# Optimization experiments

Hardware: AMD Instinct MI355X
Metric: run time of the kernel (lower is better)

The kernel has to match this reference:

```python
import jax, jax.numpy as jnp
import numpy as np

D_MODEL = 1024
N_HEADS = 16
N_KV = 4
GROUPS = N_HEADS // N_KV  # 4
D_K = D_MODEL // N_HEADS  # 64
ROPE_BASE = 10000.0
SCALE = float(np.sqrt(D_K))


def rope_cos_sin(T):
    # standard RoPE tables: [T, D_K]
    inv_freq = 1.0 / (ROPE_BASE ** (jnp.arange(0, D_K, 2, dtype=jnp.float32) / D_K))
    t = jnp.arange(T, dtype=jnp.float32)
    freqs = jnp.outer(t, inv_freq)                      # [T, D_K/2]
    emb = jnp.concatenate([freqs, freqs], axis=-1)      # [T, D_K]
    return jnp.cos(emb), jnp.sin(emb)


def apply_rope(x, cos, sin):
    # x: [B, H, T, D_K]; cos/sin: [T, D_K]
    x1, x2 = jnp.split(x, 2, axis=-1)
    rot = jnp.concatenate([-x2, x1], axis=-1)
    return x * cos[None, None] + rot * sin[None, None]


def setup_inputs() -> dict:
    key = jax.random.key(0)
    ks = jax.random.split(key, 7)
    B, T = 2, 2048
    w = lambda k, shape: jax.random.normal(k, shape, jnp.float32) * 0.02
    return {
        "q": jax.random.normal(ks[0], (B, T, D_MODEL), jnp.float32),
        "k": jax.random.normal(ks[1], (B, T, D_MODEL), jnp.float32),
        "v": jax.random.normal(ks[2], (B, T, D_MODEL), jnp.float32),
        "W_q": w(ks[3], (D_MODEL, N_HEADS * D_K)),
        "W_k": w(ks[4], (D_MODEL, N_KV * D_K)),
        "W_v": w(ks[5], (D_MODEL, N_KV * D_K)),
        "W_o": w(ks[6], (D_MODEL, D_MODEL)),
    }


def reference(q, k, v, W_q, W_k, W_v, W_o):
    B, T_q, _ = q.shape
    T_k = k.shape[1]
    # projections -> [B, H, T, D_K] (repeat_interleave == reshape heads as (kv, group))
    Q = (q @ W_q).reshape(B, T_q, N_HEADS, D_K).transpose(0, 2, 1, 3)
    K = (k @ W_k).reshape(B, T_k, N_KV, D_K).transpose(0, 2, 1, 3)
    V = (v @ W_v).reshape(B, T_k, N_KV, D_K).transpose(0, 2, 1, 3)
    cos_q, sin_q = rope_cos_sin(T_q)
    cos_k, sin_k = rope_cos_sin(T_k)
    Q = apply_rope(Q, cos_q, sin_q)
    K = apply_rope(K, cos_k, sin_k)
    # group query heads per kv head: [B, N_KV, GROUPS, T_q, D_K] (no K/V duplication)
    Qg = Q.reshape(B, N_KV, GROUPS, T_q, D_K)
    scores = jnp.einsum('bkgqd,bkld->bkgql', Qg, K) / SCALE  # [B,N_KV,G,T_q,T_k]
    attn = jax.nn.softmax(scores, axis=-1)
    out = jnp.einsum('bkgql,bkld->bkgqd', attn, V)           # [B,N_KV,G,T_q,D_K]
    out = out.reshape(B, N_HEADS, T_q, D_K).transpose(0, 2, 1, 3).reshape(B, T_q, N_HEADS * D_K)
    return out @ W_o
```

## Files before the change

kernel.cpp:

```cpp
#include <hip/hip_runtime.h>
#include <hip/hip_bf16.h>
#include <math.h>

#define B_ 2
#define T_ 2048
#define DM_ 1024
#define NH_ 16
#define NKV_ 4
#define G_ 4
#define DK_ 64
#define SCL 0.1803368784f

#define BAR_LG()                                              \
  do {                                                        \
    asm volatile("s_waitcnt lgkmcnt(0)" ::: "memory");        \
    __builtin_amdgcn_s_barrier();                             \
  } while (0)

typedef __attribute__((ext_vector_type(8))) short bf16x8;
typedef __attribute__((ext_vector_type(4))) float f32x4;
typedef __attribute__((ext_vector_type(16))) float f32x16;
typedef __attribute__((ext_vector_type(8))) unsigned short u16x8;
typedef __attribute__((ext_vector_type(4))) unsigned short u16x4;

static __device__ __forceinline__ ushort f2bf(float x) {
  __hip_bfloat16 h = __float2bfloat16(x);
  return *reinterpret_cast<ushort*>(&h);
}

__global__ __launch_bounds__(256) void prep_kernel(const float* __restrict__ Wq,
                                                   const float* __restrict__ Wk,
                                                   const float* __restrict__ Wv,
                                                   const float* __restrict__ Wo,
                                                   ushort* __restrict__ WtAll,
                                                   ushort* __restrict__ Wot,
                                                   float* __restrict__ cos_t,
                                                   float* __restrict__ sin_t) {
  const int tid = threadIdx.x;
  int bid = blockIdx.x;
  if (bid < 256) {
    int idx = bid * 256 + tid;
    int t = idx >> 5, i = idx & 31;
    float invf = 1.0f / powf(10000.0f, (float)i / 32.0f);
    float ang = (float)t * invf;
    cos_t[idx] = cosf(ang);
    sin_t[idx] = sinf(ang);
    return;
  }
  bid -= 256;
  const float* W; ushort* Wt; int N, bx, by;
  if (bid < 256)      { W = Wq; Wt = WtAll;                       N = 1024; bx = bid & 15;        by = bid >> 4; }
  else if (bid < 320) { W = Wk; Wt = WtAll + (size_t)1024 * 1024; N = 256;  bx = (bid - 256) & 3; by = (bid - 256) >> 2; }
  else if (bid < 384) { W = Wv; Wt = WtAll + (size_t)1280 * 1024; N = 256;  bx = (bid - 320) & 3; by = (bid - 320) >> 2; }
  else                { W = Wo; Wt = Wot;                         N = 1024; bx = (bid - 384) & 15; by = (bid - 384) >> 4; }
  const int n0 = bx * 64, k0 = by * 64;
  __shared__ float tile[64 * 65];
#pragma unroll
  for (int it = 0; it < 4; ++it) {
    int lin = tid + it * 256;
    int r = lin >> 4, c4 = lin & 15;
    float4 v = *(const float4*)(W + (size_t)(k0 + r) * N + n0 + c4 * 4);
    tile[r * 65 + c4 * 4 + 0] = v.x;
    tile[r * 65 + c4 * 4 + 1] = v.y;
    tile[r * 65 + c4 * 4 + 2] = v.z;
    tile[r * 65 + c4 * 4 + 3] = v.w;
  }
  __syncthreads();
#pragma unroll
  for (int it = 0; it < 4; ++it) {
    int lin = tid + it * 256;
    int n = lin >> 4, c4 = lin & 15;
    u16x4 o;
#pragma unroll
    for (int j = 0; j < 4; ++j) o[j] = f2bf(tile[(c4 * 4 + j) * 65 + n]);
    *(u16x4*)(Wt + (size_t)(n0 + n) * 1024 + k0 + c4 * 4) = o;
  }
}

__global__ __launch_bounds__(256, 2) void bgemm_kernel(const float* __restrict__ Aq,
                                                       const float* __restrict__ Ak,
                                                       const float* __restrict__ Av,
                                                       const ushort* __restrict__ Abf,
                                                       const ushort* __restrict__ Bt,
                                                       ushort* __restrict__ Qb,
                                                       ushort* __restrict__ Kb,
                                                       ushort* __restrict__ Vt,
                                                       float* __restrict__ Of, int mode,
                                                       const float* __restrict__ cos_t,
                                                       const float* __restrict__ sin_t) {
  const int tid = threadIdx.x;
  const int w = tid >> 6, lane = tid & 63;
  const int lr = lane & 15, lg = lane >> 4;
  const int wm = w >> 1, wn = w & 1;
  const int n0 = blockIdx.x * 128;
  const int m0 = blockIdx.y * 64;
  const bool f32A = (mode != 3);
  const float* Af = (n0 < 1024) ? Aq : (n0 < 1280 ? Ak : Av);

  __shared__ __align__(16) ushort As[64 * 64];
  __shared__ __align__(16) ushort Bs[128 * 64];

  f32x4 acc[2][4];
#pragma unroll
  for (int mt = 0; mt < 2; ++mt)
#pragma unroll
    for (int nt = 0; nt < 4; ++nt) acc[mt][nt] = (f32x4){0.f, 0.f, 0.f, 0.f};

  const int sr = tid >> 3, sch = tid & 7;

  float4 apf[2][2];
  u16x8 apb[2];
  u16x8 bpf[4];
  if (f32A) {
#pragma unroll
    for (int it = 0; it < 2; ++it) {
      int r = sr + it * 32;
      apf[it][0] = *(const float4*)(Af + (size_t)(m0 + r) * 1024 + sch * 8);
      apf[it][1] = *(const float4*)(Af + (size_t)(m0 + r) * 1024 + sch * 8 + 4);
    }
  } else {
#pragma unroll
    for (int it = 0; it < 2; ++it) {
      int r = sr + it * 32;
      apb[it] = *(const u16x8*)(Abf + (size_t)(m0 + r) * 1024 + sch * 8);
    }
  }
#pragma unroll
  for (int it = 0; it < 4; ++it) {
    int r = sr + it * 32;
    bpf[it] = *(const u16x8*)(Bt + (size_t)(n0 + r) * 1024 + sch * 8);
  }

  for (int kt = 0; kt < 16; ++kt) {
    BAR_LG();
#pragma unroll
    for (int it = 0; it < 2; ++it) {
      int r = sr + it * 32;
      int byte = (r * 128 + sch * 16) ^ ((r & 7) << 4);
      u16x8 aw;
      if (f32A) {
        aw[0] = f2bf(apf[it][0].x); aw[1] = f2bf(apf[it][0].y);
        aw[2] = f2bf(apf[it][0].z); aw[3] = f2bf(apf[it][0].w);
        aw[4] = f2bf(apf[it][1].x); aw[5] = f2bf(apf[it][1].y);
        aw[6] = f2bf(apf[it][1].z); aw[7] = f2bf(apf[it][1].w);
      } else {
        aw = apb[it];
      }
      *(u16x8*)((char*)As + byte) = aw;
    }
#pragma unroll
    for (int it = 0; it < 4; ++it) {
      int r = sr + it * 32;
      int byte = (r * 128 + sch * 16) ^ ((r & 7) << 4);
      *(u16x8*)((char*)Bs + byte) = bpf[it];
    }
    BAR_LG();

    if (kt + 1 < 16) {
      if (f32A) {
#pragma unroll
        for (int it = 0; it < 2; ++it) {
          int r = sr + it * 32;
          apf[it][0] = *(const float4*)(Af + (size_t)(m0 + r) * 1024 + (kt + 1) * 64 + sch * 8);
          apf[it][1] = *(const float4*)(Af + (size_t)(m0 + r) * 1024 + (kt + 1) * 64 + sch * 8 + 4);
        }
      } else {
#pragma unroll
        for (int it = 0; it < 2; ++it) {
          int r = sr + it * 32;
          apb[it] = *(const u16x8*)(Abf + (size_t)(m0 + r) * 1024 + (kt + 1) * 64 + sch * 8);
        }
      }
#pragma unroll
      for (int it = 0; it < 4; ++it) {
        int r = sr + it * 32;
        bpf[it] = *(const u16x8*)(Bt + (size_t)(n0 + r) * 1024 + (kt + 1) * 64 + sch * 8);
      }
    }

    __builtin_amdgcn_s_setprio(1);
#pragma unroll
    for (int kc = 0; kc < 2; ++kc) {
      bf16x8 af[2], bfr[4];
#pragma unroll
      for (int mt = 0; mt < 2; ++mt) {
        int row = wm * 32 + mt * 16 + lr;
        int byte = (row * 128 + kc * 64 + lg * 16) ^ ((row & 7) << 4);
        af[mt] = *(bf16x8*)((char*)As + byte);
      }
#pragma unroll
      for (int nt = 0; nt < 4; ++nt) {
        int row = wn * 64 + nt * 16 + lr;
        int byte = (row * 128 + kc * 64 + lg * 16) ^ ((row & 7) << 4);
        bfr[nt] = *(bf16x8*)((char*)Bs + byte);
      }
#pragma unroll
      for (int mt = 0; mt < 2; ++mt)
#pragma unroll
        for (int nt = 0; nt < 4; ++nt)
          acc[mt][nt] = __builtin_amdgcn_mfma_f32_16x16x32_bf16(af[mt], bfr[nt], acc[mt][nt], 0, 0, 0);
    }
    __builtin_amdgcn_s_setprio(0);
  }

  const int colbase = n0 + wn * 64;
  if (mode == 3) {
#pragma unroll
    for (int mt = 0; mt < 2; ++mt) {
      int rbase = m0 + wm * 32 + mt * 16 + lg * 4;
#pragma unroll
      for (int r = 0; r < 4; ++r)
#pragma unroll
        for (int nt = 0; nt < 4; ++nt)
          Of[(size_t)(rbase + r) * DM_ + colbase + nt * 16 + lr] = acc[mt][nt][r];
    }
  } else if (colbase >= 1280) {
    int cb = colbase - 1280;
    int kvh = cb >> 6;
#pragma unroll
    for (int mt = 0; mt < 2; ++mt) {
      int row0 = m0 + wm * 32 + mt * 16 + lg * 4;
      int b = row0 >> 11, t0r = row0 & (T_ - 1);
#pragma unroll
      for (int nt = 0; nt < 4; ++nt) {
        int d = nt * 16 + lr;
        u16x4 o;
#pragma unroll
        for (int r = 0; r < 4; ++r) o[r] = f2bf(acc[mt][nt][r]);
        *(u16x4*)(Vt + ((size_t)(b * NKV_ + kvh) * DK_ + d) * T_ + t0r) = o;
      }
    }
  } else {
    const bool isQ = (colbase < 1024);
    const int cb = isQ ? colbase : (colbase - 1024);
    const int heads = isQ ? NH_ : NKV_;
    const float scl = isQ ? SCL : 1.0f;
    const int h = cb >> 6;
    ushort* O = isQ ? Qb : Kb;
#pragma unroll
    for (int mt = 0; mt < 2; ++mt) {
      int rbase = m0 + wm * 32 + mt * 16 + lg * 4;
#pragma unroll
      for (int r = 0; r < 4; ++r) {
        int row = rbase + r;
        int b = row >> 11, t = row & (T_ - 1);
#pragma unroll
        for (int nt = 0; nt < 2; ++nt) {
          int d = nt * 16 + lr;
          float c = cos_t[t * 32 + d], s = sin_t[t * 32 + d];
          float x1 = acc[mt][nt][r], x2 = acc[mt][nt + 2][r];
          size_t base = (((size_t)(b * heads + h)) * T_ + t) * DK_ + d;
          O[base] = f2bf((x1 * c - x2 * s) * scl);
          O[base + 32] = f2bf((x2 * c + x1 * s) * scl);
        }
      }
    }
  }
}

__global__ __launch_bounds__(128, 2) void attn_mfma_kernel(const ushort* __restrict__ Qb,
                                                           const ushort* __restrict__ Kb,
                                                           const ushort* __restrict__ Vt,
                                                           ushort* __restrict__ attn_out) {
  const int bid = blockIdx.x;
  const int gw = (bid & 7) * 128 + (bid >> 3);
  const int hb = gw >> 5;
  const int qt = gw & 31;
  const int b = hb >> 4;
  const int kv = (hb >> 2) & 3;
  const int g = hb & 3;
  const int h = kv * G_ + g;
  const int q0 = qt * 64;

  const int tid = threadIdx.x;
  const int w = tid >> 6;
  const int lane = tid & 63;
  const int l31 = lane & 31;
  const int hh = lane >> 5;

  __shared__ __align__(16) ushort Ks[2][64 * 64];
  __shared__ __align__(16) ushort Vs[2][64 * 64];

  const ushort* Qg = Qb + ((size_t)(b * NH_ + h) * T_ + q0 + w * 32) * DK_;
  const ushort* Kg = Kb + (size_t)(b * NKV_ + kv) * T_ * DK_;
  const ushort* Vg = Vt + (size_t)(b * NKV_ + kv) * DK_ * T_;

  bf16x8 aq[4];
#pragma unroll
  for (int ks = 0; ks < 4; ++ks)
    aq[ks] = *(const bf16x8*)(Qg + (size_t)l31 * DK_ + ks * 16 + hh * 8);

  f32x16 oacc0{}, oacc1{};
  float l_run = 0.f;

  const int sr = tid >> 3, sch = tid & 7;
  const int vcol0b = 8 * (sch & 1) + 32 * (sch >> 1);
  u16x8 kreg[4], vreg[4];

#define LOADT(t)                                                                    \
  {                                                                                 \
    _Pragma("unroll") for (int it = 0; it < 4; ++it) {                              \
      int r = sr + it * 16;                                                         \
      kreg[it] = *(const u16x8*)(Kg + (size_t)((t) * 64 + r) * DK_ + sch * 8);      \
      vreg[it] = *(const u16x8*)(Vg + (size_t)r * T_ + (t) * 64 + sch * 8);         \
    }                                                                               \
  }
#define STAGEW(bufi)                                                                \
  {                                                                                 \
    _Pragma("unroll") for (int it = 0; it < 4; ++it) {                              \
      int r = sr + it * 16;                                                         \
      int swz = (r & 7) << 4;                                                       \
      *(u16x8*)((char*)Ks[bufi] + ((r * 128 + sch * 16) ^ swz)) = kreg[it];         \
      int vx = (r * 128 + vcol0b) ^ swz;                                            \
      u16x4 lo, hi;                                                                 \
      _Pragma("unroll") for (int j = 0; j < 4; ++j) { lo[j] = vreg[it][j]; hi[j] = vreg[it][4 + j]; } \
      *(u16x4*)((char*)Vs[bufi] + vx) = lo;                                         \
      *(u16x4*)((char*)Vs[bufi] + (vx ^ 16)) = hi;                                  \
    }                                                                               \
  }

  LOADT(0);
  STAGEW(0);
  LOADT(1);
  __syncthreads();

  const int swf = (l31 & 7) << 4;

  for (int kt = 0; kt < T_ / 64; ++kt) {
    const int cur = kt & 1;
    if (kt + 1 < T_ / 64) STAGEW(cur ^ 1);
    if (kt + 2 < T_ / 64) LOADT(kt + 2);

    f32x16 st0{}, st1{};
    __builtin_amdgcn_s_setprio(1);
#pragma unroll
    for (int ks = 0; ks < 4; ++ks) {
      bf16x8 ak0 = *(bf16x8*)((char*)Ks[cur] + ((l31 * 128 + ks * 32 + hh * 16) ^ swf));
      bf16x8 ak1 = *(bf16x8*)((char*)Ks[cur] + (((32 + l31) * 128 + ks * 32 + hh * 16) ^ swf));
      st0 = __builtin_amdgcn_mfma_f32_32x32x16_bf16(ak0, aq[ks], st0, 0, 0, 0);
      st1 = __builtin_amdgcn_mfma_f32_32x32x16_bf16(ak1, aq[ks], st1, 0, 0, 0);
    }
    __builtin_amdgcn_s_setprio(0);

    float ps = 0.f;
#pragma unroll
    for (int r = 0; r < 16; ++r) {
      st0[r] = __builtin_amdgcn_exp2f(st0[r]);
      st1[r] = __builtin_amdgcn_exp2f(st1[r]);
      ps += st0[r] + st1[r];
    }
    l_run += ps;

    __builtin_amdgcn_s_setprio(1);
#pragma unroll
    for (int s = 0; s < 4; ++s) {
      const int base = (s & 1) * 8;
      u16x8 pw;
#pragma unroll
      for (int j = 0; j < 8; ++j)
        pw[j] = f2bf((s < 2) ? st0[base + j] : st1[base + j]);
      bf16x8 pa = *(bf16x8*)&pw;
      bf16x8 bv0 = *(bf16x8*)((char*)Vs[cur] + ((l31 * 128 + s * 32 + hh * 16) ^ swf));
      bf16x8 bv1 = *(bf16x8*)((char*)Vs[cur] + (((32 + l31) * 128 + s * 32 + hh * 16) ^ swf));
      oacc0 = __builtin_amdgcn_mfma_f32_32x32x16_bf16(pa, bv0, oacc0, 0, 0, 0);
      oacc1 = __builtin_amdgcn_mfma_f32_32x32x16_bf16(pa, bv1, oacc1, 0, 0, 0);
    }
    __builtin_amdgcn_s_setprio(0);

    __syncthreads();
  }

  float l_tot = l_run + __shfl_xor(l_run, 32, 64);
  float inv = 1.0f / l_tot;
#pragma unroll
  for (int r = 0; r < 16; ++r) {
    int qr = (r & 3) + 8 * (r >> 2) + 4 * hh;
    float ir = __shfl(inv, qr, 64);
    int t = q0 + w * 32 + qr;
    size_t base = ((size_t)b * T_ + t) * DM_ + h * DK_;
    attn_out[base + l31] = f2bf(oacc0[r] * ir);
    attn_out[base + 32 + l31] = f2bf(oacc1[r] * ir);
  }
#undef LOADT
#undef STAGEW
}

extern "C" void kernel_launch(void* const* d_in, const int* in_sizes, int n_in,
                              void* d_out, int out_size, void* d_ws, size_t ws_size,
                              hipStream_t stream) {
  const float* q  = (const float*)d_in[0];
  const float* k  = (const float*)d_in[1];
  const float* v  = (const float*)d_in[2];
  const float* Wq = (const float*)d_in[3];
  const float* Wk = (const float*)d_in[4];
  const float* Wv = (const float*)d_in[5];
  const float* Wo = (const float*)d_in[6];
  float* out = (float*)d_out;

  char* ws = (char*)d_ws;
  size_t off = 0;
  float* cos_t  = (float*)(ws + off);  off += (size_t)T_ * 32 * 4;
  float* sin_t  = (float*)(ws + off);  off += (size_t)T_ * 32 * 4;
  ushort* Ab    = (ushort*)(ws + off); off += (size_t)4096 * 1024 * 2;
  ushort* WtAll = (ushort*)(ws + off); off += (size_t)1536 * 1024 * 2;
  ushort* Wot   = (ushort*)(ws + off); off += (size_t)1024 * 1024 * 2;
  ushort* Qb    = (ushort*)(ws + off); off += (size_t)B_ * NH_ * T_ * DK_ * 2;
  ushort* Kb    = (ushort*)(ws + off); off += (size_t)B_ * NKV_ * T_ * DK_ * 2;
  ushort* Vt    = (ushort*)(ws + off); off += (size_t)B_ * NKV_ * T_ * DK_ * 2;

  prep_kernel<<<dim3(896), dim3(256), 0, stream>>>(Wq, Wk, Wv, Wo, WtAll, Wot, cos_t, sin_t);

  bgemm_kernel<<<dim3(12, 64), dim3(256), 0, stream>>>(q, k, v, nullptr, WtAll,
                                                       Qb, Kb, Vt, nullptr, 5, cos_t, sin_t);

  attn_mfma_kernel<<<dim3(1024), dim3(128), 0, stream>>>(Qb, Kb, Vt, Ab);

  bgemm_kernel<<<dim3(8, 64), dim3(256), 0, stream>>>(nullptr, nullptr, nullptr, Ab, Wot,
                                                      nullptr, nullptr, nullptr, out, 3, cos_t, sin_t);
}
```

Baseline: 112.8 us.

## Stream GEMM B tiles and attention K/V tiles directly into LDS via global_load_lds

Replaces the register-staged global→LDS copies with asynchronous global_load_lds (direct-to-LDS) loads. This applies to the weight tile in the projection GEMM, now double-buffered, and to the K/V tiles in the attention kernel. The XOR swizzle on those LDS buffers is dropped, since direct loads write contiguous rows. The V-transpose store permutes its lane groups so the memory layout matches the un-swizzled read pattern. The aim is to cut VGPR pressure and VALU/ds_write work for staging. The cost is possible LDS bank conflicts on reads and a shallower prefetch depth in attention (one tile instead of two).

```diff
diff --git a/kernel.cpp b/kernel.cpp
--- a/kernel.cpp
+++ b/kernel.cpp
@@ -16,6 +16,11 @@
     asm volatile("s_waitcnt lgkmcnt(0)" ::: "memory");        \
     __builtin_amdgcn_s_barrier();                             \
   } while (0)
+
+#define GLOAD16(gp, lp)                                                      \
+  __builtin_amdgcn_global_load_lds(                                          \
+      (const __attribute__((address_space(1))) unsigned int*)(gp),           \
+      (__attribute__((address_space(3))) unsigned int*)(lp), 16, 0, 0)
 
 typedef __attribute__((ext_vector_type(8))) short bf16x8;
 typedef __attribute__((ext_vector_type(4))) float f32x4;
@@ -96,9 +101,10 @@
   const int m0 = blockIdx.y * 64;
   const bool f32A = (mode != 3);
   const float* Af = (n0 < 1024) ? Aq : (n0 < 1280 ? Ak : Av);
+  const int krow8 = lane >> 3, kch = lane & 7;
 
   __shared__ __align__(16) ushort As[64 * 64];
-  __shared__ __align__(16) ushort Bs[128 * 64];
+  __shared__ __align__(16) ushort Bs[2][128 * 64];
 
   f32x4 acc[2][4];
 #pragma unroll
@@ -107,10 +113,16 @@
     for (int nt = 0; nt < 4; ++nt) acc[mt][nt] = (f32x4){0.f, 0.f, 0.f, 0.f};
 
   const int sr = tid >> 3, sch = tid & 7;
+
+#define ISSUE_B(bufi, t)                                                          \
+  {                                                                               \
+    _Pragma("unroll") for (int i = 0; i < 4; ++i)                                 \
+      GLOAD16(Bt + (size_t)(n0 + w * 32 + i * 8 + krow8) * 1024 + (t) * 64 + kch * 8, \
+              (char*)Bs[bufi] + (w * 32 + i * 8) * 128);                          \
+  }
 
   float4 apf[2][2];
   u16x8 apb[2];
-  u16x8 bpf[4];
   if (f32A) {
 #pragma unroll
     for (int it = 0; it < 2; ++it) {
@@ -125,14 +137,12 @@
       apb[it] = *(const u16x8*)(Abf + (size_t)(m0 + r) * 1024 + sch * 8);
     }
   }
-#pragma unroll
-  for (int it = 0; it < 4; ++it) {
-    int r = sr + it * 32;
-    bpf[it] = *(const u16x8*)(Bt + (size_t)(n0 + r) * 1024 + sch * 8);
-  }
+  ISSUE_B(0, 0);
 
   for (int kt = 0; kt < 16; ++kt) {
-    BAR_LG();
+    const int cur = kt & 1;
+    __syncthreads();
+    if (kt + 1 < 16) ISSUE_B(cur ^ 1, kt + 1);
 #pragma unroll
     for (int it = 0; it < 2; ++it) {
       int r = sr + it * 32;
@@ -148,12 +158,6 @@
       }
       *(u16x8*)((char*)As + byte) = aw;
     }
-#pragma unroll
-    for (int it = 0; it < 4; ++it) {
-      int r = sr + it * 32;
-      int byte = (r * 128 + sch * 16) ^ ((r & 7) << 4);
-      *(u16x8*)((char*)Bs + byte) = bpf[it];
-    }
     BAR_LG();
 
     if (kt + 1 < 16) {
@@ -171,11 +175,6 @@
           apb[it] = *(const u16x8*)(Abf + (size_t)(m0 + r) * 1024 + (kt + 1) * 64 + sch * 8);
         }
       }
-#pragma unroll
-      for (int it = 0; it < 4; ++it) {
-        int r = sr + it * 32;
-        bpf[it] = *(const u16x8*)(Bt + (size_t)(n0 + r) * 1024 + (kt + 1) * 64 + sch * 8);
-      }
     }
 
     __builtin_amdgcn_s_setprio(1);
@@ -191,8 +190,7 @@
 #pragma unroll
       for (int nt = 0; nt < 4; ++nt) {
         int row = wn * 64 + nt * 16 + lr;
-        int byte = (row * 128 + kc * 64 + lg * 16) ^ ((row & 7) << 4);
-        bfr[nt] = *(bf16x8*)((char*)Bs + byte);
+        bfr[nt] = *(bf16x8*)((char*)Bs[cur] + row * 128 + kc * 64 + lg * 16);
       }
 #pragma unroll
       for (int mt = 0; mt < 2; ++mt)
@@ -202,6 +200,7 @@
     }
     __builtin_amdgcn_s_setprio(0);
   }
+#undef ISSUE_B
 
   const int colbase = n0 + wn * 64;
   if (mode == 3) {
@@ -215,11 +214,11 @@
           Of[(size_t)(rbase + r) * DM_ + colbase + nt * 16 + lr] = acc[mt][nt][r];
     }
   } else if (colbase >= 1280) {
-    int cb = colbase - 1280;
-    int kvh = cb >> 6;
+    int kvh = (colbase - 1280) >> 6;
+    const int lgp = ((lg & 1) << 1) | (lg >> 1);
 #pragma unroll
     for (int mt = 0; mt < 2; ++mt) {
-      int row0 = m0 + wm * 32 + mt * 16 + lg * 4;
+      int row0 = m0 + wm * 32 + mt * 16 + lgp * 4;
       int b = row0 >> 11, t0r = row0 & (T_ - 1);
 #pragma unroll
       for (int nt = 0; nt < 4; ++nt) {
@@ -277,6 +276,7 @@
   const int lane = tid & 63;
   const int l31 = lane & 31;
   const int hh = lane >> 5;
+  const int krow8 = lane >> 3, kch = lane & 7;
 
   __shared__ __align__(16) ushort Ks[2][64 * 64];
   __shared__ __align__(16) ushort Vs[2][64 * 64];
@@ -293,50 +293,29 @@
   f32x16 oacc0{}, oacc1{};
   float l_run = 0.f;
 
-  const int sr = tid >> 3, sch = tid & 7;
-  const int vcol0b = 8 * (sch & 1) + 32 * (sch >> 1);
-  u16x8 kreg[4], vreg[4];
-
-#define LOADT(t)                                                                    \
+#define ISSUE(bufi, t)                                                              \
   {                                                                                 \
-    _Pragma("unroll") for (int it = 0; it < 4; ++it) {                              \
-      int r = sr + it * 16;                                                         \
-      kreg[it] = *(const u16x8*)(Kg + (size_t)((t) * 64 + r) * DK_ + sch * 8);      \
-      vreg[it] = *(const u16x8*)(Vg + (size_t)r * T_ + (t) * 64 + sch * 8);         \
+    _Pragma("unroll") for (int i = 0; i < 4; ++i) {                                 \
+      GLOAD16(Kg + (size_t)((t) * 64 + w * 32 + i * 8 + krow8) * DK_ + kch * 8,     \
+              (char*)Ks[bufi] + (w * 32 + i * 8) * 128);                            \
+      GLOAD16(Vg + (size_t)(w * 32 + i * 8 + krow8) * T_ + (t) * 64 + kch * 8,      \
+              (char*)Vs[bufi] + (w * 32 + i * 8) * 128);                            \
     }                                                                               \
   }
-#define STAGEW(bufi)                                                                \
-  {                                                                                 \
-    _Pragma("unroll") for (int it = 0; it < 4; ++it) {                              \
-      int r = sr + it * 16;                                                         \
-      int swz = (r & 7) << 4;                                                       \
-      *(u16x8*)((char*)Ks[bufi] + ((r * 128 + sch * 16) ^ swz)) = kreg[it];         \
-      int vx = (r * 128 + vcol0b) ^ swz;                                            \
-      u16x4 lo, hi;                                                                 \
-      _Pragma("unroll") for (int j = 0; j < 4; ++j) { lo[j] = vreg[it][j]; hi[j] = vreg[it][4 + j]; } \
-      *(u16x4*)((char*)Vs[bufi] + vx) = lo;                                         \
-      *(u16x4*)((char*)Vs[bufi] + (vx ^ 16)) = hi;                                  \
-    }                                                                               \
-  }
-
-  LOADT(0);
-  STAGEW(0);
-  LOADT(1);
+
+  ISSUE(0, 0);
   __syncthreads();
-
-  const int swf = (l31 & 7) << 4;
 
   for (int kt = 0; kt < T_ / 64; ++kt) {
     const int cur = kt & 1;
-    if (kt + 1 < T_ / 64) STAGEW(cur ^ 1);
-    if (kt + 2 < T_ / 64) LOADT(kt + 2);
+    if (kt + 1 < T_ / 64) ISSUE(cur ^ 1, kt + 1);
 
     f32x16 st0{}, st1{};
     __builtin_amdgcn_s_setprio(1);
 #pragma unroll
     for (int ks = 0; ks < 4; ++ks) {
-      bf16x8 ak0 = *(bf16x8*)((char*)Ks[cur] + ((l31 * 128 + ks * 32 + hh * 16) ^ swf));
-      bf16x8 ak1 = *(bf16x8*)((char*)Ks[cur] + (((32 + l31) * 128 + ks * 32 + hh * 16) ^ swf));
+      bf16x8 ak0 = *(bf16x8*)((char*)Ks[cur] + l31 * 128 + ks * 32 + hh * 16);
+      bf16x8 ak1 = *(bf16x8*)((char*)Ks[cur] + (32 + l31) * 128 + ks * 32 + hh * 16);
       st0 = __builtin_amdgcn_mfma_f32_32x32x16_bf16(ak0, aq[ks], st0, 0, 0, 0);
       st1 = __builtin_amdgcn_mfma_f32_32x32x16_bf16(ak1, aq[ks], st1, 0, 0, 0);
     }
@@ -360,8 +339,8 @@
       for (int j = 0; j < 8; ++j)
         pw[j] = f2bf((s < 2) ? st0[base + j] : st1[base + j]);
       bf16x8 pa = *(bf16x8*)&pw;
-      bf16x8 bv0 = *(bf16x8*)((char*)Vs[cur] + ((l31 * 128 + s * 32 + hh * 16) ^ swf));
-      bf16x8 bv1 = *(bf16x8*)((char*)Vs[cur] + (((32 + l31) * 128 + s * 32 + hh * 16) ^ swf));
+      bf16x8 bv0 = *(bf16x8*)((char*)Vs[cur] + l31 * 128 + s * 32 + hh * 16);
+      bf16x8 bv1 = *(bf16x8*)((char*)Vs[cur] + (32 + l31) * 128 + s * 32 + hh * 16);
       oacc0 = __builtin_amdgcn_mfma_f32_32x32x16_bf16(pa, bv0, oacc0, 0, 0, 0);
       oacc1 = __builtin_amdgcn_mfma_f32_32x32x16_bf16(pa, bv1, oacc1, 0, 0, 0);
     }
@@ -369,6 +348,7 @@
 
     __syncthreads();
   }
+#undef ISSUE
 
   float l_tot = l_run + __shfl_xor(l_run, 32, 64);
   float inv = 1.0f / l_tot;
@@ -381,8 +361,6 @@
     attn_out[base + l31] = f2bf(oacc0[r] * ir);
     attn_out[base + 32 + l31] = f2bf(oacc1[r] * ir);
   }
-#undef LOADT
-#undef STAGEW
 }
 
 extern "C" void kernel_launch(void* const* d_in, const int* in_sizes, int n_in,
```

After: 130.6 us. 15.7% more time.
